# Kernel optimization log

Measured on AMD Instinct MI355X. Metric: run time of the kernel, lower is better.

Reference implementation:

```python
import jax, jax.numpy as jnp
import numpy as np

D_INPUT = 1024
N_HEADS = 16
D_INNER = 64
SEQ = 1024
PREV = 1024
BS = 4
LN_EPS = 1e-5


def _rel_shift(x):
    # x: (i, j, b, h) -> Transformer-XL relative shift trick
    i, j, b, h = x.shape
    zero_pad = jnp.zeros((i, 1, b, h), dtype=x.dtype)
    return jnp.concatenate([zero_pad, x], axis=1).reshape(j + 1, i, b, h)[1:].reshape(i, j, b, h)


def setup_inputs() -> dict:
    key = jax.random.key(0)
    ks = jax.random.split(key, 9)
    w = 0.02
    return {
        "input_": jax.random.normal(ks[0], (SEQ, BS, D_INPUT), jnp.float32),
        "pos_embs": jax.random.normal(ks[1], (SEQ + PREV, D_INPUT), jnp.float32),
        "memory": jax.random.normal(ks[2], (PREV, BS, D_INPUT), jnp.float32),
        "u": jax.random.normal(ks[3], (N_HEADS, D_INNER), jnp.float32) * w,
        "v": jax.random.normal(ks[4], (N_HEADS, D_INNER), jnp.float32) * w,
        "W_kv": jax.random.normal(ks[5], (D_INPUT, 2 * N_HEADS * D_INNER), jnp.float32) * w,
        "W_q": jax.random.normal(ks[6], (D_INPUT, N_HEADS * D_INNER), jnp.float32) * w,
        "W_p": jax.random.normal(ks[7], (D_INPUT, N_HEADS * D_INNER), jnp.float32) * w,
        "W_out": jax.random.normal(ks[8], (N_HEADS * D_INNER, D_INPUT), jnp.float32) * w,
        "ln_g": jnp.ones((D_INPUT,), jnp.float32),
        "ln_b": jnp.zeros((D_INPUT,), jnp.float32),
    }


def reference(input_, pos_embs, memory, u, v, W_kv, W_q, W_p, W_out, ln_g, ln_b):
    S, B, D = input_.shape
    P = memory.shape[0]
    T = S + P
    H, d = u.shape
    scale = 1.0 / (d ** 0.5)

    x_mem = jnp.concatenate([memory, input_], axis=0)          # (T, B, D)
    kv = x_mem @ W_kv                                          # (T, B, 2*H*d)
    k, val = jnp.split(kv, 2, axis=-1)
    k = k.reshape(T, B, H, d)
    val = val.reshape(T, B, H, d)
    q = (input_ @ W_q).reshape(S, B, H, d)                     # (S, B, H, d)

    content_attn = jnp.einsum('ibhd,jbhd->ijbh', q + u, k)     # (S, T, B, H)
    p = (pos_embs @ W_p).reshape(T, H, d)                      # (T, H, d)
    position_attn = jnp.einsum('ibhd,jhd->ijbh', q + v, p)     # (S, T, B, H)
    position_attn = _rel_shift(position_attn)

    attn = jax.nn.softmax((content_attn + position_attn) * scale, axis=1)
    awv = jnp.einsum('ijbh,jbhd->ibhd', attn, val).reshape(S, B, H * d)

    out = input_ + awv @ W_out                                 # residual
    mu = jnp.mean(out, axis=-1, keepdims=True)
    var = jnp.mean(jnp.square(out - mu), axis=-1, keepdims=True)
    return (out - mu) * jax.lax.rsqrt(var + LN_EPS) * ln_g + ln_b
```

## Files before the change

kernel.cpp:

```cpp
#include <hip/hip_runtime.h>
#include <cstdint>
#include <cstddef>

#define S_  1024
#define B_  4
#define T_  2048
#define H_  16

typedef short     short8 __attribute__((ext_vector_type(8)));
typedef float     f32x4  __attribute__((ext_vector_type(4)));
typedef unsigned short u16x8 __attribute__((ext_vector_type(8)));

__device__ __forceinline__ unsigned short f2b(float f){
  uint32_t x = __builtin_bit_cast(uint32_t, f);
  x = (x + 0x7fffu + ((x >> 16) & 1u)) >> 16;
  return (unsigned short)x;
}
__device__ __forceinline__ unsigned short f2bt(float f){
  return (unsigned short)(__builtin_bit_cast(uint32_t, f) >> 16);
}
__device__ __forceinline__ float b2f(unsigned short u){
  return __builtin_bit_cast(float, ((uint32_t)u) << 16);
}

__device__ __forceinline__ void gl_lds16(const unsigned short* g, unsigned short* l){
  __builtin_amdgcn_global_load_lds(
      (const __attribute__((address_space(1))) void*)g,
      (__attribute__((address_space(3))) void*)l,
      16, 0, 0);
}

__global__ __launch_bounds__(256) void cvt_cat(
    const float* __restrict__ a, const float* __restrict__ bsrc,
    int splitElems, int total, unsigned short* __restrict__ out)
{
  int i = (blockIdx.x * 256 + threadIdx.x) * 4;
  if (i >= total) return;
  const float* src = (i < splitElems) ? (a + i) : (bsrc + (i - splitElems));
  float4 x = *(const float4*)src;
  ushort4 o;
  o.x = f2b(x.x); o.y = f2b(x.y); o.z = f2b(x.z); o.w = f2b(x.w);
  *(ushort4*)(out + i) = o;
}

__global__ __launch_bounds__(256) void wtrans(
    const float* __restrict__ in, unsigned short* __restrict__ out, int R, int C)
{
  __shared__ float tile[32][33];
  const int R0 = blockIdx.y * 32, C0 = blockIdx.x * 32;
  const int t = threadIdx.x;
  const int r = t >> 3, c4 = (t & 7) * 4;
  float4 x = *(const float4*)(in + (size_t)(R0 + r) * C + C0 + c4);
  tile[r][c4+0] = x.x; tile[r][c4+1] = x.y; tile[r][c4+2] = x.z; tile[r][c4+3] = x.w;
  __syncthreads();
  ushort4 o;
  o.x = f2b(tile[c4+0][r]); o.y = f2b(tile[c4+1][r]);
  o.z = f2b(tile[c4+2][r]); o.w = f2b(tile[c4+3][r]);
  *(ushort4*)(out + (size_t)(C0 + r) * R + R0 + c4) = o;
}

__global__ __launch_bounds__(256) void vtrans(
    const unsigned short* __restrict__ kvb, unsigned short* __restrict__ vtg)
{
  __shared__ __align__(16) unsigned short tile[64][72];
  const int t = threadIdx.x;
  const int bh = blockIdx.y;
  const int b = bh >> 4, h = bh & 15;
  const int t0 = blockIdx.x * 64;
  #pragma unroll
  for (int l = 0; l < 2; ++l){
    int idx = t + l * 256;
    int row = idx >> 3, seg = (idx & 7) * 8;
    u16x8 x = *(const u16x8*)(kvb + ((size_t)(t0 + row) * 4 + b) * 2048 + 1024 + h * 64 + seg);
    *(u16x8*)&tile[row][seg] = x;
  }
  __syncthreads();
  #pragma unroll
  for (int l = 0; l < 2; ++l){
    int idx = t + l * 256;
    int d = idx >> 3, nseg = (idx & 7) * 8;
    u16x8 o;
    #pragma unroll
    for (int j = 0; j < 8; ++j) o[j] = tile[nseg + j][d];
    *(u16x8*)(vtg + ((size_t)bh * 64 + d) * 2048 + t0 + nseg) = o;
  }
}

#define AS_IDX(row,k) ((((row) >> 3) * 512) + (((k) >> 3) * 64) + (((row) & 7) * 8) + ((k) & 7))

__global__ __launch_bounds__(256) void gemm_multi(
    const unsigned short* __restrict__ xb,
    const unsigned short* __restrict__ posb,
    const unsigned short* __restrict__ WkvT,
    const unsigned short* __restrict__ WqT,
    const unsigned short* __restrict__ WpT,
    unsigned short* __restrict__ kvb,
    unsigned short* __restrict__ qbb,
    unsigned short* __restrict__ pbb)
{
  const unsigned short *A, *BT;
  unsigned short* C;
  int N, local;
  int bx = (blockIdx.x & 7) * 176 + (blockIdx.x >> 3);
  if (bx < 1024){       A = xb;                       BT = WkvT; C = kvb; N = 2048; local = bx;        }
  else if (bx < 1280){  A = xb + (size_t)4096 * 1024; BT = WqT;  C = qbb; N = 1024; local = bx - 1024; }
  else {                A = posb;                     BT = WpT;  C = pbb; N = 1024; local = bx - 1280; }
  const int nb = N >> 7;
  const int M0 = (local / nb) * 128, N0 = (local % nb) * 128;
  const int K = 1024;

  __shared__ __align__(16) unsigned short As[128 * 64];
  __shared__ __align__(16) unsigned short Bs[128 * 64];
  const int t = threadIdx.x;
  const int w = t >> 6, lane = t & 63, quad = lane >> 4, l16 = lane & 15;
  const int wm = (w >> 1) * 64, wn = (w & 1) * 64;
  const int lr = lane & 7, lcb = lane >> 3;

  f32x4 acc[4][4] = {};

  for (int k0 = 0; k0 < K; k0 += 64){
    __syncthreads();
    #pragma unroll
    for (int i = 0; i < 4; ++i){
      int blk = 4 * w + i;
      gl_lds16(A  + (size_t)(M0 + 8 * blk + lr) * K + k0 + lcb * 8, As + blk * 512);
      gl_lds16(BT + (size_t)(N0 + 8 * blk + lr) * K + k0 + lcb * 8, Bs + blk * 512);
    }
    __syncthreads();
    #pragma unroll
    for (int ks = 0; ks < 2; ++ks){
      short8 af[4], bf[4];
      #pragma unroll
      for (int rt = 0; rt < 4; ++rt)
        af[rt] = *(short8*)&As[AS_IDX(wm + rt * 16 + l16, ks * 32 + quad * 8)];
      #pragma unroll
      for (int ct = 0; ct < 4; ++ct)
        bf[ct] = *(short8*)&Bs[AS_IDX(wn + ct * 16 + l16, ks * 32 + quad * 8)];
      #pragma unroll
      for (int rt = 0; rt < 4; ++rt)
        #pragma unroll
        for (int ct = 0; ct < 4; ++ct)
          acc[rt][ct] = __builtin_amdgcn_mfma_f32_16x16x32_bf16(af[rt], bf[ct], acc[rt][ct], 0, 0, 0);
    }
  }

  #pragma unroll
  for (int rt = 0; rt < 4; ++rt)
    #pragma unroll
    for (int r = 0; r < 4; ++r){
      int row = M0 + wm + rt * 16 + quad * 4 + r;
      #pragma unroll
      for (int ct = 0; ct < 4; ++ct)
        C[(size_t)row * N + N0 + wn + ct * 16 + l16] = f2b(acc[rt][ct][r]);
    }
}

__global__ __launch_bounds__(256) void gemm_outk(
    const unsigned short* __restrict__ A,
    const unsigned short* __restrict__ BT,
    float* __restrict__ OutP)
{
  const int K = 1024, N = 1024;
  int lid = blockIdx.x + 8 * (blockIdx.y + 32 * blockIdx.z);
  int sw  = (lid & 7) * 64 + (lid >> 3);
  const int N0 = (sw & 7) * 128;
  const int M0 = ((sw >> 3) & 31) * 128;
  const int kz = sw >> 8;
  const int k0s = kz * 512, k0e = k0s + 512;
  float* outF = OutP + (size_t)kz * 4096 * 1024;

  __shared__ __align__(16) unsigned short As[128 * 64];
  __shared__ __align__(16) unsigned short Bs[128 * 64];
  const int t = threadIdx.x;
  const int w = t >> 6, lane = t & 63, quad = lane >> 4, l16 = lane & 15;
  const int wm = (w >> 1) * 64, wn = (w & 1) * 64;
  const int lr = lane & 7, lcb = lane >> 3;

  f32x4 acc[4][4] = {};

  for (int k0 = k0s; k0 < k0e; k0 += 64){
    __syncthreads();
    #pragma unroll
    for (int i = 0; i < 4; ++i){
      int blk = 4 * w + i;
      gl_lds16(A  + (size_t)(M0 + 8 * blk + lr) * K + k0 + lcb * 8, As + blk * 512);
      gl_lds16(BT + (size_t)(N0 + 8 * blk + lr) * K + k0 + lcb * 8, Bs + blk * 512);
    }
    __syncthreads();
    #pragma unroll
    for (int ks = 0; ks < 2; ++ks){
      short8 af[4], bf[4];
      #pragma unroll
      for (int rt = 0; rt < 4; ++rt)
        af[rt] = *(short8*)&As[AS_IDX(wm + rt * 16 + l16, ks * 32 + quad * 8)];
      #pragma unroll
      for (int ct = 0; ct < 4; ++ct)
        bf[ct] = *(short8*)&Bs[AS_IDX(wn + ct * 16 + l16, ks * 32 + quad * 8)];
      #pragma unroll
      for (int rt = 0; rt < 4; ++rt)
        #pragma unroll
        for (int ct = 0; ct < 4; ++ct)
          acc[rt][ct] = __builtin_amdgcn_mfma_f32_16x16x32_bf16(af[rt], bf[ct], acc[rt][ct], 0, 0, 0);
    }
  }

  #pragma unroll
  for (int rt = 0; rt < 4; ++rt)
    #pragma unroll
    for (int r = 0; r < 4; ++r){
      int row = M0 + wm + rt * 16 + quad * 4 + r;
      #pragma unroll
      for (int ct = 0; ct < 4; ++ct)
        outF[(size_t)row * N + N0 + wn + ct * 16 + l16] = acc[rt][ct][r];
    }
}

#define SP_IX(gm,n) ((gm) * 64 + ((n) ^ (((gm) & 12) << 2)))

__global__ __launch_bounds__(256, 3) void attn_mfma(
    const unsigned short* __restrict__ qb,
    const unsigned short* __restrict__ kvb,
    const unsigned short* __restrict__ pbm,
    const unsigned short* __restrict__ vtg,
    const float* __restrict__ ub, const float* __restrict__ vb,
    unsigned short* __restrict__ opart,
    float* __restrict__ lpart)
{
  __shared__ __align__(16) unsigned short Kc[64 * 64];
  __shared__ __align__(16) unsigned short VT[64 * 64];
  __shared__ __align__(16) unsigned short Pw[128 * 64];
  __shared__ __align__(16) unsigned short SP[64 * 64];

  const int t = threadIdx.x;
  int lin = blockIdx.x + 16 * (blockIdx.y + 64 * blockIdx.z);
  int swz = (lin & 7) * 256 + (lin >> 3);
  const int i0 = (swz & 15) * 64;
  const int bh = (swz >> 4) & 63;
  const int jh = swz >> 10;
  const int b = bh >> 4, h = bh & 15;
  const int w = t >> 6, lane = t & 63, quad = lane >> 4, l16 = lane & 15;
  const int colbase = h * 64 + quad * 8;
  const int ctLo = 3 - w;

  const float SCQ = 0.1803368801f;
  const float EOF_ = 23.0831206f;

  short8 qu[2], qv[2][2];
  #pragma unroll
  for (int cs = 0; cs < 2; ++cs){
    int gr = i0 + 16 * w + l16 + cs;
    #pragma unroll
    for (int ks = 0; ks < 2; ++ks){
      u16x8 q8 = *(const u16x8*)(qb + ((size_t)gr * 4 + b) * 1024 + colbase + ks * 32);
      #pragma unroll
      for (int j = 0; j < 8; ++j){
        float f = b2f(q8[j]);
        qv[cs][ks][j] = (short)f2b((f + vb[colbase + ks * 32 + j]) * SCQ);
        if (cs == 0) qu[ks][j] = (short)f2b((f + ub[colbase + ks * 32 + j]) * SCQ);
      }
    }
  }

  f32x4 oacc[4] = {};
  float lsum[4] = {0.f, 0.f, 0.f, 0.f};

  u16x8 pk[2], pv2[2], pp[4];

  auto loadKV = [&](int jc){
    const int j0 = jc * 64;
    #pragma unroll
    for (int l = 0; l < 2; ++l){
      int idx = t + l * 256;
      int row = idx >> 3, cb = idx & 7;
      pk[l]  = *(const u16x8*)(kvb + ((size_t)(j0 + row) * 4 + b) * 2048 + h * 64 + cb * 8);
      pv2[l] = *(const u16x8*)(vtg + ((size_t)bh * 64 + row) * 2048 + j0 + cb * 8);
    }
  };

  auto loadPPfull = [&](int jc){
    const int D = jc * 64 - i0;
    #pragma unroll
    for (int l = 0; l < 4; ++l){
      int idx = t + l * 256;
      int row = idx >> 3, cb = idx & 7;
      int pr;
      if (D <= 960)          pr = D + 960 + row;
      else if (D == 1024)    pr = (row < 64) ? (1984 + row) : (row - 65);
      else                   pr = D - 1089 + row;
      u16x8 x;
      if (pr >= 0 && pr < T_){
        x = *(const u16x8*)(pbm + (size_t)pr * 1024 + h * 64 + cb * 8);
      } else {
        for (int j = 0; j < 8; ++j) x[j] = 0;
      }
      pp[l] = x;
    }
  };

  auto loadPPhalf = [&](int jc){
    const int D = jc * 64 - i0;
    #pragma unroll
    for (int l = 0; l < 2; ++l){
      int idx = t + l * 256;
      int rowh = idx >> 3, cb = idx & 7;
      int pr = (D <= 960) ? (D + 1024 + rowh) : (D - 1025 + rowh);
      u16x8 x;
      if (pr >= 0 && pr < T_){
        x = *(const u16x8*)(pbm + (size_t)pr * 1024 + h * 64 + cb * 8);
      } else {
        for (int j = 0; j < 8; ++j) x[j] = 0;
      }
      pp[l] = x;
    }
  };

  auto storeKV = [&](){
    #pragma unroll
    for (int l = 0; l < 2; ++l){
      int idx = t + l * 256;
      int row = idx >> 3, cb = idx & 7;
      int sw = (cb ^ (row & 7)) * 8;
      *(u16x8*)&Kc[row * 64 + sw] = pk[l];
      *(u16x8*)&VT[row * 64 + sw] = pv2[l];
    }
  };
  auto storePPfull = [&](){
    #pragma unroll
    for (int l = 0; l < 4; ++l){
      int idx = t + l * 256;
      int row = idx >> 3, cb = idx & 7;
      *(u16x8*)&Pw[row * 64 + ((cb ^ (row & 7)) * 8)] = pp[l];
    }
  };
  auto storePPhalf = [&](int physh){
    #pragma unroll
    for (int l = 0; l < 2; ++l){
      int idx = t + l * 256;
      int rowh = idx >> 3, cb = idx & 7;
      *(u16x8*)&Pw[(physh * 64 + rowh) * 64 + ((cb ^ (rowh & 7)) * 8)] = pp[l];
    }
  };

  const int jcs = jh * 16, jce = jcs + 16;
  loadKV(jcs);
  loadPPfull(jcs);
  int par = 0;

  #pragma unroll 1
  for (int jc = jcs; jc < jce; ++jc){
    const int D = jc * 64 - i0;

    __syncthreads();
    storeKV();
    if (jc == jcs) storePPfull(); else storePPhalf(1 ^ par);
    if (jc + 1 < jce){ loadKV(jc + 1); loadPPhalf(jc + 1); }
    __syncthreads();

    #pragma unroll
    for (int ci = 0; ci < 5; ++ci){
      int ct = ctLo + ci;
      int cs = (D <= 960) ? 0 : ((D >= 1088) ? 1 : ((ct >= 4) ? 1 : 0));
      f32x4 racc = {};
      #pragma unroll
      for (int ks = 0; ks < 2; ++ks){
        int rr = ct * 16 + l16;
        int prow = ((rr >> 6) ^ par) * 64 + (rr & 63);
        short8 bf = *(short8*)&Pw[prow * 64 + (((ks * 4 + quad) ^ (rr & 7)) * 8)];
        racc = __builtin_amdgcn_mfma_f32_16x16x32_bf16(qv[cs][ks], bf, racc, 0, 0, 0);
      }
      int c = ct * 16 + l16;
      #pragma unroll
      for (int r = 0; r < 4; ++r){
        int gm = 16 * w + quad * 4 + r;
        int n = c + gm - 63;
        if ((unsigned)n < 64u) SP[SP_IX(gm, n)] = f2bt(racc[r]);
      }
    }

    f32x4 cacc[4] = {};
    #pragma unroll
    for (int ks = 0; ks < 2; ++ks){
      #pragma unroll
      for (int ct = 0; ct < 4; ++ct){
        int rr = ct * 16 + l16;
        short8 bf = *(short8*)&Kc[rr * 64 + (((ks * 4 + quad) ^ (rr & 7)) * 8)];
        cacc[ct] = __builtin_amdgcn_mfma_f32_16x16x32_bf16(qu[ks], bf, cacc[ct], 0, 0, 0);
      }
    }

    #pragma unroll
    for (int ct = 0; ct < 4; ++ct){
      #pragma unroll
      for (int r = 0; r < 4; ++r){
        int gm = 16 * w + quad * 4 + r;
        int n = ct * 16 + l16;
        int ix = SP_IX(gm, n);
        float s = cacc[ct][r] + b2f(SP[ix]);
        float e = __builtin_amdgcn_exp2f(s - EOF_);
        lsum[r] += e;
        SP[ix] = f2bt(e);
      }
    }

    #pragma unroll
    for (int ks = 0; ks < 2; ++ks){
      short8 af = *(short8*)&SP[SP_IX(16 * w + l16, ks * 32 + quad * 8)];
      #pragma unroll
      for (int dt = 0; dt < 4; ++dt){
        int rr = dt * 16 + l16;
        short8 bf = *(short8*)&VT[rr * 64 + (((ks * 4 + quad) ^ (rr & 7)) * 8)];
        oacc[dt] = __builtin_amdgcn_mfma_f32_16x16x32_bf16(af, bf, oacc[dt], 0, 0, 0);
      }
    }

    par ^= 1;
  }

  unsigned short* ob = opart + (size_t)jh * 4096 * 1024;
  float* lb = lpart + (size_t)jh * 4096 * 16;
  #pragma unroll
  for (int r = 0; r < 4; ++r){
    float red = lsum[r];
    #pragma unroll
    for (int mk = 1; mk < 16; mk <<= 1)
      red += __shfl_xor(red, mk, 64);
    int srow = i0 + 16 * w + quad * 4 + r;
    int grow = srow * 4 + b;
    #pragma unroll
    for (int dt = 0; dt < 4; ++dt)
      ob[(size_t)grow * 1024 + h * 64 + dt * 16 + l16] = f2bt(oacc[dt][r]);
    if (l16 == 0) lb[(size_t)grow * 16 + h] = red;
  }
}

__global__ __launch_bounds__(256) void attn_combine(
    const unsigned short* __restrict__ opart, const float* __restrict__ lpart,
    unsigned short* __restrict__ awvb)
{
  const int grow = blockIdx.x, t = threadIdx.x;
  const int d4 = t * 4, h = t >> 4;
  float l = lpart[(size_t)grow * 16 + h] + lpart[(size_t)4096 * 16 + grow * 16 + h];
  float inv = 1.f / l;
  ushort4 a = *(const ushort4*)(opart + (size_t)grow * 1024 + d4);
  ushort4 c = *(const ushort4*)(opart + (size_t)4096 * 1024 + grow * 1024 + d4);
  ushort4 o;
  o.x = f2bt((b2f(a.x) + b2f(c.x)) * inv);
  o.y = f2bt((b2f(a.y) + b2f(c.y)) * inv);
  o.z = f2bt((b2f(a.z) + b2f(c.z)) * inv);
  o.w = f2bt((b2f(a.w) + b2f(c.w)) * inv);
  *(ushort4*)(awvb + (size_t)grow * 1024 + d4) = o;
}

__global__ __launch_bounds__(256) void ln2_kernel(
    const float* __restrict__ inp, const float* __restrict__ OutP,
    const float* __restrict__ g, const float* __restrict__ bb,
    float* __restrict__ out)
{
  const int row = blockIdx.x, t = threadIdx.x;
  float4 x  = *(const float4*)(inp  + (size_t)row * 1024 + t * 4);
  float4 p0 = *(const float4*)(OutP + (size_t)row * 1024 + t * 4);
  float4 p1 = *(const float4*)(OutP + (size_t)4096 * 1024 + row * 1024 + t * 4);
  x.x += p0.x + p1.x; x.y += p0.y + p1.y; x.z += p0.z + p1.z; x.w += p0.w + p1.w;
  float s  = x.x + x.y + x.z + x.w;
  float s2 = x.x*x.x + x.y*x.y + x.z*x.z + x.w*x.w;
  #pragma unroll
  for (int o = 32; o > 0; o >>= 1){
    s  += __shfl_down(s, o);
    s2 += __shfl_down(s2, o);
  }
  __shared__ float rs[4], rs2[4];
  int w = t >> 6, lane = t & 63;
  if (lane == 0){ rs[w] = s; rs2[w] = s2; }
  __syncthreads();
  s  = rs[0] + rs[1] + rs[2] + rs[3];
  s2 = rs2[0] + rs2[1] + rs2[2] + rs2[3];
  float mu   = s * (1.f/1024.f);
  float var  = s2 * (1.f/1024.f) - mu*mu;
  float rstd = rsqrtf(var + 1e-5f);
  float4 gg = *(const float4*)(g + t*4);
  float4 bv = *(const float4*)(bb + t*4);
  float4 o;
  o.x = (x.x - mu)*rstd*gg.x + bv.x;
  o.y = (x.y - mu)*rstd*gg.y + bv.y;
  o.z = (x.z - mu)*rstd*gg.z + bv.z;
  o.w = (x.w - mu)*rstd*gg.w + bv.w;
  *(float4*)(out + (size_t)row * 1024 + t * 4) = o;
}

extern "C" void kernel_launch(void* const* d_in, const int* in_sizes, int n_in,
                              void* d_out, int out_size, void* d_ws, size_t ws_size,
                              hipStream_t stream) {
  (void)in_sizes; (void)n_in; (void)out_size; (void)ws_size;
  const float* input_ = (const float*)d_in[0];
  const float* pos    = (const float*)d_in[1];
  const float* mem    = (const float*)d_in[2];
  const float* u      = (const float*)d_in[3];
  const float* v      = (const float*)d_in[4];
  const float* Wkv    = (const float*)d_in[5];
  const float* Wq     = (const float*)d_in[6];
  const float* Wp     = (const float*)d_in[7];
  const float* Wout   = (const float*)d_in[8];
  const float* lng    = (const float*)d_in[9];
  const float* lnb    = (const float*)d_in[10];
  float* out = (float*)d_out;

  unsigned short* ws   = (unsigned short*)d_ws;
  unsigned short* xb    = ws;
  unsigned short* posb  = xb    + (size_t)8192*1024;
  unsigned short* WkvT  = posb  + (size_t)2048*1024;
  unsigned short* WqT   = WkvT  + (size_t)2048*1024;
  unsigned short* WpT   = WqT   + (size_t)1024*1024;
  unsigned short* WoutT = WpT   + (size_t)1024*1024;
  unsigned short* kvb   = WoutT + (size_t)1024*1024;
  unsigned short* qbb   = kvb   + (size_t)8192*2048;
  unsigned short* pbb   = qbb   + (size_t)4096*1024;
  unsigned short* vtg   = pbb   + (size_t)2048*1024;
  unsigned short* awvb  = vtg   + (size_t)4096*2048;

  unsigned short* opart = xb;
  float*          lpart = (float*)posb;
  float*          OutP  = (float*)kvb;

  cvt_cat<<<8192, 256, 0, stream>>>(mem, input_, 4096*1024, 8192*1024, xb);
  cvt_cat<<<2048, 256, 0, stream>>>(pos, pos, 2048*1024, 2048*1024, posb);
  wtrans<<<dim3(64, 32), 256, 0, stream>>>(Wkv,  WkvT, 1024, 2048);
  wtrans<<<dim3(32, 32), 256, 0, stream>>>(Wq,   WqT,  1024, 1024);
  wtrans<<<dim3(32, 32), 256, 0, stream>>>(Wp,   WpT,  1024, 1024);
  wtrans<<<dim3(32, 32), 256, 0, stream>>>(Wout, WoutT,1024, 1024);

  gemm_multi<<<1408, 256, 0, stream>>>(xb, posb, WkvT, WqT, WpT, kvb, qbb, pbb);

  vtrans<<<dim3(32, 64), 256, 0, stream>>>(kvb, vtg);

  attn_mfma<<<dim3(16, 64, 2), 256, 0, stream>>>(qbb, kvb, pbb, vtg, u, v, opart, lpart);
  attn_combine<<<4096, 256, 0, stream>>>(opart, lpart, awvb);

  gemm_outk<<<dim3(8, 32, 2), 256, 0, stream>>>(awvb, WoutT, OutP);
  ln2_kernel<<<4096, 256, 0, stream>>>(input_, OutP, lng, lnb, out);
}
```

Before: 424.8 us.

## Drop attention split-K, normalize in-kernel, and merge conversion launches

The attention kernel no longer splits the key range into two halves with a separate combine pass. Each block now walks all 32 key chunks and normalizes its output by the row sum before writing bf16 directly, which removes the partial-output writes and the combine kernel. The grid shrinks from 2048 to 1024 blocks, so there is less parallelism and fewer waves on the GPU. Separately, the two input conversion launches and four weight transpose launches are merged into one launch each to cut launch overhead.

```diff
diff --git a/kernel.cpp b/kernel.cpp
--- a/kernel.cpp
+++ b/kernel.cpp
@@ -30,24 +30,45 @@
       16, 0, 0);
 }
 
-__global__ __launch_bounds__(256) void cvt_cat(
-    const float* __restrict__ a, const float* __restrict__ bsrc,
-    int splitElems, int total, unsigned short* __restrict__ out)
+__global__ __launch_bounds__(256) void cvt_all(
+    const float* __restrict__ memsrc, const float* __restrict__ inp,
+    const float* __restrict__ pos,
+    unsigned short* __restrict__ xb, unsigned short* __restrict__ posb)
 {
   int i = (blockIdx.x * 256 + threadIdx.x) * 4;
-  if (i >= total) return;
-  const float* src = (i < splitElems) ? (a + i) : (bsrc + (i - splitElems));
+  const float* src;
+  unsigned short* dst;
+  if (i < 8192 * 1024){
+    src = (i < 4096 * 1024) ? (memsrc + i) : (inp + (i - 4096 * 1024));
+    dst = xb + i;
+  } else {
+    int i2 = i - 8192 * 1024;
+    src = pos + i2;
+    dst = posb + i2;
+  }
   float4 x = *(const float4*)src;
   ushort4 o;
   o.x = f2b(x.x); o.y = f2b(x.y); o.z = f2b(x.z); o.w = f2b(x.w);
-  *(ushort4*)(out + i) = o;
-}
-
-__global__ __launch_bounds__(256) void wtrans(
-    const float* __restrict__ in, unsigned short* __restrict__ out, int R, int C)
+  *(ushort4*)dst = o;
+}
+
+__global__ __launch_bounds__(256) void wtrans_all(
+    const float* __restrict__ Wkv, const float* __restrict__ Wq,
+    const float* __restrict__ Wp,  const float* __restrict__ Wout,
+    unsigned short* __restrict__ WkvT, unsigned short* __restrict__ WqT,
+    unsigned short* __restrict__ WpT,  unsigned short* __restrict__ WoutT)
 {
   __shared__ float tile[32][33];
-  const int R0 = blockIdx.y * 32, C0 = blockIdx.x * 32;
+  int blk = blockIdx.x;
+  const float* in; unsigned short* out; int C, bx, by;
+  if (blk < 2048){ in = Wkv; out = WkvT; C = 2048; bx = blk & 63; by = blk >> 6; }
+  else {
+    int r = blk - 2048; int wi = r >> 10; r &= 1023;
+    C = 1024; bx = r & 31; by = r >> 5;
+    in  = (wi == 0) ? Wq  : ((wi == 1) ? Wp  : Wout);
+    out = (wi == 0) ? WqT : ((wi == 1) ? WpT : WoutT);
+  }
+  const int R0 = by * 32, C0 = bx * 32;
   const int t = threadIdx.x;
   const int r = t >> 3, c4 = (t & 7) * 4;
   float4 x = *(const float4*)(in + (size_t)(R0 + r) * C + C0 + c4);
@@ -56,7 +77,7 @@
   ushort4 o;
   o.x = f2b(tile[c4+0][r]); o.y = f2b(tile[c4+1][r]);
   o.z = f2b(tile[c4+2][r]); o.w = f2b(tile[c4+3][r]);
-  *(ushort4*)(out + (size_t)(C0 + r) * R + R0 + c4) = o;
+  *(ushort4*)(out + (size_t)(C0 + r) * 1024 + R0 + c4) = o;
 }
 
 __global__ __launch_bounds__(256) void vtrans(
@@ -223,8 +244,7 @@
     const unsigned short* __restrict__ pbm,
     const unsigned short* __restrict__ vtg,
     const float* __restrict__ ub, const float* __restrict__ vb,
-    unsigned short* __restrict__ opart,
-    float* __restrict__ lpart)
+    unsigned short* __restrict__ awvb)
 {
   __shared__ __align__(16) unsigned short Kc[64 * 64];
   __shared__ __align__(16) unsigned short VT[64 * 64];
@@ -232,11 +252,8 @@
   __shared__ __align__(16) unsigned short SP[64 * 64];
 
   const int t = threadIdx.x;
-  int lin = blockIdx.x + 16 * (blockIdx.y + 64 * blockIdx.z);
-  int swz = (lin & 7) * 256 + (lin >> 3);
-  const int i0 = (swz & 15) * 64;
-  const int bh = (swz >> 4) & 63;
-  const int jh = swz >> 10;
+  const int i0 = blockIdx.x * 64;
+  const int bh = blockIdx.y;
   const int b = bh >> 4, h = bh & 15;
   const int w = t >> 6, lane = t & 63, quad = lane >> 4, l16 = lane & 15;
   const int colbase = h * 64 + quad * 8;
@@ -341,19 +358,18 @@
     }
   };
 
-  const int jcs = jh * 16, jce = jcs + 16;
-  loadKV(jcs);
-  loadPPfull(jcs);
+  loadKV(0);
+  loadPPfull(0);
   int par = 0;
 
   #pragma unroll 1
-  for (int jc = jcs; jc < jce; ++jc){
+  for (int jc = 0; jc < 32; ++jc){
     const int D = jc * 64 - i0;
 
     __syncthreads();
     storeKV();
-    if (jc == jcs) storePPfull(); else storePPhalf(1 ^ par);
-    if (jc + 1 < jce){ loadKV(jc + 1); loadPPhalf(jc + 1); }
+    if (jc == 0) storePPfull(); else storePPhalf(1 ^ par);
+    if (jc + 1 < 32){ loadKV(jc + 1); loadPPhalf(jc + 1); }
     __syncthreads();
 
     #pragma unroll
@@ -416,39 +432,19 @@
     par ^= 1;
   }
 
-  unsigned short* ob = opart + (size_t)jh * 4096 * 1024;
-  float* lb = lpart + (size_t)jh * 4096 * 16;
   #pragma unroll
   for (int r = 0; r < 4; ++r){
     float red = lsum[r];
     #pragma unroll
     for (int mk = 1; mk < 16; mk <<= 1)
       red += __shfl_xor(red, mk, 64);
+    float inv = 1.f / red;
     int srow = i0 + 16 * w + quad * 4 + r;
     int grow = srow * 4 + b;
     #pragma unroll
     for (int dt = 0; dt < 4; ++dt)
-      ob[(size_t)grow * 1024 + h * 64 + dt * 16 + l16] = f2bt(oacc[dt][r]);
-    if (l16 == 0) lb[(size_t)grow * 16 + h] = red;
-  }
-}
-
-__global__ __launch_bounds__(256) void attn_combine(
-    const unsigned short* __restrict__ opart, const float* __restrict__ lpart,
-    unsigned short* __restrict__ awvb)
-{
-  const int grow = blockIdx.x, t = threadIdx.x;
-  const int d4 = t * 4, h = t >> 4;
-  float l = lpart[(size_t)grow * 16 + h] + lpart[(size_t)4096 * 16 + grow * 16 + h];
-  float inv = 1.f / l;
-  ushort4 a = *(const ushort4*)(opart + (size_t)grow * 1024 + d4);
-  ushort4 c = *(const ushort4*)(opart + (size_t)4096 * 1024 + grow * 1024 + d4);
-  ushort4 o;
-  o.x = f2bt((b2f(a.x) + b2f(c.x)) * inv);
-  o.y = f2bt((b2f(a.y) + b2f(c.y)) * inv);
-  o.z = f2bt((b2f(a.z) + b2f(c.z)) * inv);
-  o.w = f2bt((b2f(a.w) + b2f(c.w)) * inv);
-  *(ushort4*)(awvb + (size_t)grow * 1024 + d4) = o;
+      awvb[(size_t)grow * 1024 + h * 64 + dt * 16 + l16] = f2bt(oacc[dt][r] * inv);
+  }
 }
 
 __global__ __launch_bounds__(256) void ln2_kernel(
@@ -517,23 +513,16 @@
   unsigned short* vtg   = pbb   + (size_t)2048*1024;
   unsigned short* awvb  = vtg   + (size_t)4096*2048;
 
-  unsigned short* opart = xb;
-  float*          lpart = (float*)posb;
-  float*          OutP  = (float*)kvb;
-
-  cvt_cat<<<8192, 256, 0, stream>>>(mem, input_, 4096*1024, 8192*1024, xb);
-  cvt_cat<<<2048, 256, 0, stream>>>(pos, pos, 2048*1024, 2048*1024, posb);
-  wtrans<<<dim3(64, 32), 256, 0, stream>>>(Wkv,  WkvT, 1024, 2048);
-  wtrans<<<dim3(32, 32), 256, 0, stream>>>(Wq,   WqT,  1024, 1024);
-  wtrans<<<dim3(32, 32), 256, 0, stream>>>(Wp,   WpT,  1024, 1024);
-  wtrans<<<dim3(32, 32), 256, 0, stream>>>(Wout, WoutT,1024, 1024);
+  float* OutP = (float*)kvb;
+
+  cvt_all<<<10240, 256, 0, stream>>>(mem, input_, pos, xb, posb);
+  wtrans_all<<<5120, 256, 0, stream>>>(Wkv, Wq, Wp, Wout, WkvT, WqT, WpT, WoutT);
 
   gemm_multi<<<1408, 256, 0, stream>>>(xb, posb, WkvT, WqT, WpT, kvb, qbb, pbb);
 
   vtrans<<<dim3(32, 64), 256, 0, stream>>>(kvb, vtg);
 
-  attn_mfma<<<dim3(16, 64, 2), 256, 0, stream>>>(qbb, kvb, pbb, vtg, u, v, opart, lpart);
-  attn_combine<<<4096, 256, 0, stream>>>(opart, lpart, awvb);
+  attn_mfma<<<dim3(16, 64), 256, 0, stream>>>(qbb, kvb, pbb, vtg, u, v, awvb);
 
   gemm_outk<<<dim3(8, 32, 2), 256, 0, stream>>>(awvb, WoutT, OutP);
   ln2_kernel<<<4096, 256, 0, stream>>>(input_, OutP, lng, lnb, out);
```

Result: faster. 414.1 us (-2.5%).
